# Optimization experiments

Hardware: AMD Instinct MI355X
Metric: run time of the kernel (lower is better)

## Reference

```python
import jax, jax.numpy as jnp
import numpy as np

BIT_DEPTH = 8  # feature squeezing

def setup_inputs() -> dict:
    key = jax.random.key(0)
    ks = jax.random.split(key, 8)
    B, C, H, W = 8, 256, 64, 64
    Cq = C // 8
    x = jax.random.normal(ks[0], (B, C, H, W), dtype=jnp.float32)
    # 1x1 conv weights stored as [out, in] (kernel dims squeezed)
    wq = jax.random.normal(ks[1], (Cq, C), dtype=jnp.float32) * 0.05
    bq = jax.random.normal(ks[2], (Cq,), dtype=jnp.float32) * 0.05
    wk = jax.random.normal(ks[3], (Cq, C), dtype=jnp.float32) * 0.05
    bk = jax.random.normal(ks[4], (Cq,), dtype=jnp.float32) * 0.05
    wv = jax.random.normal(ks[5], (C, C), dtype=jnp.float32) * 0.05
    bv = jax.random.normal(ks[6], (C,), dtype=jnp.float32) * 0.05
    gamma = jax.random.normal(ks[7], (1,), dtype=jnp.float32) * 0.1
    return {"x": x, "wq": wq, "bq": bq, "wk": wk, "bk": bk, "wv": wv, "bv": bv, "gamma": gamma}

def reference(x, wq, bq, wk, bk, wv, bv, gamma):
    B, C, H, W = x.shape
    N = H * W
    xf = x.reshape(B, C, N)  # flatten spatial
    # 1x1 convs == per-pixel linear projections
    q = jnp.einsum('bcn,oc->bon', xf, wq) + bq[None, :, None]   # [B, C/8, N]
    k = jnp.einsum('bcn,oc->bon', xf, wk) + bk[None, :, None]   # [B, C/8, N]
    v = jnp.einsum('bcn,oc->bon', xf, wv) + bv[None, :, None]   # [B, C, N]
    energy = jnp.einsum('bcn,bcm->bnm', q, k)                   # [B, N, N] (no scaling, as in source)
    attn = jax.nn.softmax(energy, axis=-1)
    out = jnp.einsum('bcm,bnm->bcn', v, attn).reshape(B, C, H, W)
    out = gamma[0] * out + out               # gamma-scaled residual of attention output
    scale = jnp.float32(2 ** BIT_DEPTH)
    return jnp.floor(out * scale) / scale    # feature squeezing (bit_depth=8)
```

## Files before the change

kernel.cpp:

```cpp
#include <hip/hip_runtime.h>
#include <math.h>

namespace {
constexpr int BB = 8;
constexpr int CH = 256;
constexpr int CQ = 32;
constexpr int NN = 4096;
}

typedef float f32x4 __attribute__((ext_vector_type(4)));
typedef short bf16x8 __attribute__((ext_vector_type(8)));
typedef unsigned short us8 __attribute__((ext_vector_type(8)));

#define MFMA16(a, b, c) __builtin_amdgcn_mfma_f32_16x16x32_bf16(a, b, c, 0, 0, 0)

__device__ __forceinline__ unsigned short f2bf(float x) {
    unsigned int u = __float_as_uint(x);
    u += 0x7fffu + ((u >> 16) & 1u);
    return (unsigned short)(u >> 16);
}
__device__ __forceinline__ float bf2f(unsigned short h) {
    return __uint_as_float(((unsigned int)h) << 16);
}
__device__ __forceinline__ void gload16(const void* g, void* l) {
    __builtin_amdgcn_global_load_lds(
        (const __attribute__((address_space(1))) unsigned int*)g,
        (__attribute__((address_space(3))) unsigned int*)l, 16, 0, 0);
}

__global__ __launch_bounds__(256) void wsplit_kernel(
    const float* __restrict__ wq, const float* __restrict__ wk,
    const float* __restrict__ wv,
    unsigned short* __restrict__ wh, unsigned short* __restrict__ wl)
{
    int idx = blockIdx.x * 256 + threadIdx.x;
    float v;
    if (idx < 8192)       v = wq[idx];
    else if (idx < 16384) v = wk[idx - 8192];
    else                  v = wv[idx - 16384];
    unsigned short hi = f2bf(v);
    wh[idx] = hi;
    wl[idx] = f2bf(v - bf2f(hi));
}

__global__ __launch_bounds__(256) void transpose_kernel(
    const float* __restrict__ x,
    unsigned short* __restrict__ xh, unsigned short* __restrict__ xl)
{
    __shared__ float xf[64 * 68];
    __shared__ unsigned short hs[64 * 80];
    __shared__ unsigned short ls[64 * 80];
    const int t  = threadIdx.x;
    const int b  = blockIdx.x >> 8;
    const int tl = blockIdx.x & 255;
    const int c0 = (tl >> 6) * 64;
    const int n0 = (tl & 63) * 64;

    #pragma unroll
    for (int i = 0; i < 4; ++i) {
        int idx = i * 256 + t;
        int c = idx >> 4, nf = idx & 15;
        float4 v4 = *(const float4*)(x + ((size_t)(b * 256 + c0 + c)) * NN + n0 + nf * 4);
        *(float4*)(xf + c * 68 + nf * 4) = v4;
    }
    __syncthreads();

    const int n = t & 63;
    #pragma unroll
    for (int loop = 0; loop < 2; ++loop) {
        int chunk = (t >> 6) + 4 * loop;
        us8 h8, l8;
        #pragma unroll
        for (int j = 0; j < 8; ++j) {
            float v = xf[(chunk * 8 + j) * 68 + n];
            unsigned short hi = f2bf(v);
            h8[j] = hi;
            l8[j] = f2bf(v - bf2f(hi));
        }
        *(us8*)(hs + n * 80 + chunk * 8) = h8;
        *(us8*)(ls + n * 80 + chunk * 8) = l8;
    }
    __syncthreads();

    {
        int rn = t >> 2, piece = t & 3;
        size_t grow = ((size_t)(b * NN + n0 + rn)) * 256 + c0 + piece * 16;
        *(us8*)(xh + grow)     = *(const us8*)(hs + rn * 80 + piece * 16);
        *(us8*)(xh + grow + 8) = *(const us8*)(hs + rn * 80 + piece * 16 + 8);
        *(us8*)(xl + grow)     = *(const us8*)(ls + rn * 80 + piece * 16);
        *(us8*)(xl + grow + 8) = *(const us8*)(ls + rn * 80 + piece * 16 + 8);
    }
}

#define PJ_XL 32768
#define PJ_VE 16384
__global__ __launch_bounds__(256, 2) void proj_kernel(
    const unsigned short* __restrict__ xh, const unsigned short* __restrict__ xl,
    const unsigned short* __restrict__ wh, const unsigned short* __restrict__ wl,
    const float* __restrict__ bq, const float* __restrict__ bk,
    const float* __restrict__ bv,
    unsigned short* __restrict__ qh, unsigned short* __restrict__ ql,
    unsigned short* __restrict__ kh, unsigned short* __restrict__ kl,
    unsigned short* __restrict__ vt)
{
    __shared__ __align__(16) unsigned char smem[65536];
    const int t    = threadIdx.x;
    const int lane = t & 63;
    const int w    = t >> 6;
    const int l16  = lane & 15;
    const int quad = lane >> 4;
    const int b    = blockIdx.x >> 6;
    const int n0   = (blockIdx.x & 63) << 6;

    const unsigned char* xhB = (const unsigned char*)(xh + ((size_t)b * NN + n0) * 256);
    const unsigned char* xlB = (const unsigned char*)(xl + ((size_t)b * NN + n0) * 256);
    #pragma unroll
    for (int j = 0; j < 8; ++j) {
        int idx = j * 256 + t;
        int r = idx >> 5, cl = idx & 31;
        int cg = cl ^ (r & 7);
        gload16(xhB + (size_t)r * 512 + cg * 16, smem + idx * 16);
        gload16(xlB + (size_t)r * 512 + cg * 16, smem + PJ_XL + idx * 16);
    }
    __syncthreads();

    f32x4 acc[5][4] = {};
    #pragma unroll 1
    for (int kc = 0; kc < 8; ++kc) {
        bf16x8 ah[5], al[5];
        #pragma unroll
        for (int i = 0; i < 5; ++i) {
            int och = (w * 5 + i) * 16 + l16;
            ah[i] = *(const bf16x8*)(wh + och * 256 + kc * 32 + quad * 8);
            al[i] = *(const bf16x8*)(wl + och * 256 + kc * 32 + quad * 8);
        }
        #pragma unroll
        for (int nt = 0; nt < 4; ++nt) {
            int roff = (nt * 16 + l16) * 512 + (((kc * 4 + quad) ^ (l16 & 7)) * 16);
            bf16x8 bh = *(const bf16x8*)(smem + roff);
            bf16x8 bl = *(const bf16x8*)(smem + PJ_XL + roff);
            #pragma unroll
            for (int i = 0; i < 5; ++i) {
                acc[i][nt] = MFMA16(ah[i], bh, acc[i][nt]);
                acc[i][nt] = MFMA16(al[i], bh, acc[i][nt]);
                acc[i][nt] = MFMA16(ah[i], bl, acc[i][nt]);
            }
        }
    }
    __syncthreads();

    #pragma unroll
    for (int i = 0; i < 5; ++i) {
        int tile = w * 5 + i;
        if (tile < 4) {
            #pragma unroll
            for (int r = 0; r < 4; ++r) {
                int och = tile * 16 + quad * 4 + r;
                float bias = (och < 32) ? bq[och] : bk[och - 32];
                int arr = (och < 32) ? 0 : 2;
                int oq = och & 31;
                #pragma unroll
                for (int nt = 0; nt < 4; ++nt) {
                    float val = acc[i][nt][r] + bias;
                    unsigned short hi = f2bf(val);
                    unsigned short lo = f2bf(val - bf2f(hi));
                    *(unsigned short*)(smem + arr * 4096 + (nt * 16 + l16) * 64 + oq * 2) = hi;
                    *(unsigned short*)(smem + (arr + 1) * 4096 + (nt * 16 + l16) * 64 + oq * 2) = lo;
                }
            }
        } else {
            #pragma unroll
            for (int r = 0; r < 4; ++r) {
                int voch = tile * 16 + quad * 4 + r - 64;
                float bias = bv[voch];
                #pragma unroll
                for (int nt = 0; nt < 4; ++nt) {
                    *(unsigned short*)(smem + PJ_VE + voch * 136 + (nt * 16 + l16) * 2)
                        = f2bf(acc[i][nt][r] + bias);
                }
            }
        }
    }
    __syncthreads();

    {
        unsigned short* dsts[4] = { qh, ql, kh, kl };
        int arr = t >> 6, n = t & 63;
        unsigned short* dst = dsts[arr] + ((size_t)b * NN + n0 + n) * 32;
        #pragma unroll
        for (int i = 0; i < 4; ++i)
            *(us8*)(dst + i * 8) = *(const us8*)(smem + arr * 4096 + n * 64 + i * 16);
    }
    #pragma unroll
    for (int p = 0; p < 4; ++p) {
        int voch = p * 64 + (t >> 2), piece = t & 3;
        unsigned short* dst = vt + ((size_t)b * CH + voch) * NN + n0 + piece * 16;
        *(us8*)(dst)     = *(const us8*)(smem + PJ_VE + voch * 136 + piece * 32);
        *(us8*)(dst + 8) = *(const us8*)(smem + PJ_VE + voch * 136 + piece * 32 + 16);
    }
}

#define A_P0 0
#define A_P1 8192
#define A_V0 16384
#define A_V1 49152
#define A_SM 16384

__global__ __launch_bounds__(256, 2) void attn_kernel(
    const unsigned short* __restrict__ qh, const unsigned short* __restrict__ ql,
    const unsigned short* __restrict__ kh, const unsigned short* __restrict__ kl,
    const unsigned short* __restrict__ vt, const float* __restrict__ gptr,
    float* __restrict__ out)
{
    __shared__ __align__(16) unsigned char smem[81920];
    const int t    = threadIdx.x;
    const int lane = t & 63;
    const int w    = t >> 6;
    const int l16  = lane & 15;
    const int quad = lane >> 4;
    const int b    = blockIdx.x & 7;
    const int n0   = (blockIdx.x >> 3) << 6;

    bf16x8 qhA[4], qlA[4];
    #pragma unroll
    for (int qt = 0; qt < 4; ++qt) {
        size_t row = (size_t)b * NN + n0 + qt * 16 + l16;
        qhA[qt] = *(const bf16x8*)(qh + row * 32 + quad * 8);
        qlA[qt] = *(const bf16x8*)(ql + row * 32 + quad * 8);
    }

    const unsigned short* khbase = kh + ((size_t)b * NN + w * 16 + l16) * 32 + quad * 8;
    const unsigned short* klbase = kl + ((size_t)b * NN + w * 16 + l16) * 32 + quad * 8;
    const unsigned char*  vtB    = (const unsigned char*)(vt + (size_t)b * CH * NN);

    f32x4 acc[4][4] = {};
    float S[4][4] = {};

    bf16x8 kch = *(const bf16x8*)(khbase);
    bf16x8 kcl = *(const bf16x8*)(klbase);
    #pragma unroll
    for (int j = 0; j < 8; ++j) {
        int idx = j * 256 + t;
        int r = idx >> 3, cl = idx & 7;
        int cg = cl ^ (r & 7);
        gload16(vtB + (size_t)r * 8192 + cg * 16, smem + A_V0 + idx * 16);
    }

    #pragma unroll 1
    for (int tile = 0; tile < 64; ++tile) {
        unsigned char* P = smem + ((tile & 1) ? A_P1 : A_P0);
        const int key = w * 16 + l16;
        #pragma unroll
        for (int qt = 0; qt < 4; ++qt) {
            f32x4 e = { 0.f, 0.f, 0.f, 0.f };
            e = MFMA16(qhA[qt], kch, e);
            e = MFMA16(qlA[qt], kch, e);
            e = MFMA16(qhA[qt], kcl, e);
            #pragma unroll
            for (int r = 0; r < 4; ++r) {
                float p = __expf(e[r]);
                unsigned short pb = f2bf(p);
                S[qt][r] += bf2f(pb);
                int row = qt * 16 + quad * 4 + r;
                *(unsigned short*)(P + row * 128
                                     + ((((key >> 3) ^ (row & 7)) << 4)
                                        | ((key & 7) << 1))) = pb;
            }
        }

        __syncthreads();

        const int m1 = ((tile + 1) & 63) * 64;
        bf16x8 knh = *(const bf16x8*)(khbase + (size_t)m1 * 32);
        bf16x8 knl = *(const bf16x8*)(klbase + (size_t)m1 * 32);
        if (tile < 63) {
            unsigned char* vdst = smem + ((tile & 1) ? A_V0 : A_V1);
            const unsigned char* vsrc = vtB + (size_t)m1 * 2;
            #pragma unroll
            for (int j = 0; j < 8; ++j) {
                int idx = j * 256 + t;
                int r = idx >> 3, cl = idx & 7;
                int cg = cl ^ (r & 7);
                gload16(vsrc + (size_t)r * 8192 + cg * 16, vdst + idx * 16);
            }
        }

        const unsigned char* VB = smem + ((tile & 1) ? A_V1 : A_V0);
        #pragma unroll
        for (int ks = 0; ks < 2; ++ks) {
            bf16x8 af[4], bfr[4];
            #pragma unroll
            for (int qt = 0; qt < 4; ++qt) {
                int row = qt * 16 + l16;
                af[qt] = *(const bf16x8*)(P + row * 128
                                            + (((ks * 4 + quad) ^ (row & 7)) << 4));
            }
            #pragma unroll
            for (int ct = 0; ct < 4; ++ct) {
                int vrow = w * 64 + ct * 16 + l16;
                int ch = (ks * 4 + quad) ^ (l16 & 7);
                bfr[ct] = *(const bf16x8*)(VB + vrow * 128 + ch * 16);
            }
            __builtin_amdgcn_s_setprio(1);
            #pragma unroll
            for (int qt = 0; qt < 4; ++qt)
                #pragma unroll
                for (int ct = 0; ct < 4; ++ct)
                    acc[qt][ct] = MFMA16(af[qt], bfr[ct], acc[qt][ct]);
            __builtin_amdgcn_s_setprio(0);
        }
        kch = knh;
        kcl = knl;
    }

    #pragma unroll
    for (int mask = 1; mask <= 8; mask <<= 1)
        #pragma unroll
        for (int qt = 0; qt < 4; ++qt)
            #pragma unroll
            for (int r = 0; r < 4; ++r)
                S[qt][r] += __shfl_xor(S[qt][r], mask);
    float* SM = (float*)(smem + A_SM);
    if (l16 == 0) {
        #pragma unroll
        for (int qt = 0; qt < 4; ++qt)
            #pragma unroll
            for (int r = 0; r < 4; ++r)
                SM[w * 64 + qt * 16 + quad * 4 + r] = S[qt][r];
    }
    __syncthreads();

    const float g1 = 1.f + gptr[0];
    float* ob = out + (size_t)b * CH * NN;
    #pragma unroll
    for (int qt = 0; qt < 4; ++qt) {
        float is[4];
        #pragma unroll
        for (int r = 0; r < 4; ++r) {
            int qi = qt * 16 + quad * 4 + r;
            float Sf = SM[qi] + SM[64 + qi] + SM[128 + qi] + SM[192 + qi];
            is[r] = g1 / Sf;
        }
        #pragma unroll
        for (int ct = 0; ct < 4; ++ct) {
            float4 o4;
            o4.x = floorf(acc[qt][ct][0] * is[0] * 256.f) * 0.00390625f;
            o4.y = floorf(acc[qt][ct][1] * is[1] * 256.f) * 0.00390625f;
            o4.z = floorf(acc[qt][ct][2] * is[2] * 256.f) * 0.00390625f;
            o4.w = floorf(acc[qt][ct][3] * is[3] * 256.f) * 0.00390625f;
            *(float4*)(ob + (size_t)(w * 64 + ct * 16 + l16) * NN
                          + n0 + qt * 16 + quad * 4) = o4;
        }
    }
}

extern "C" void kernel_launch(void* const* d_in, const int* in_sizes, int n_in,
                              void* d_out, int out_size, void* d_ws, size_t ws_size,
                              hipStream_t stream) {
    const float* x  = (const float*)d_in[0];
    const float* wq = (const float*)d_in[1];
    const float* bq = (const float*)d_in[2];
    const float* wk = (const float*)d_in[3];
    const float* bk = (const float*)d_in[4];
    const float* wv = (const float*)d_in[5];
    const float* bv = (const float*)d_in[6];
    const float* gm = (const float*)d_in[7];
    float* out = (float*)d_out;

    unsigned short* ws = (unsigned short*)d_ws;
    const size_t XSZ = (size_t)BB * NN * 256;
    const size_t WSZ = 320 * 256;
    const size_t QSZ = (size_t)BB * NN * 32;
    unsigned short* xh = ws;
    unsigned short* xl = xh + XSZ;
    unsigned short* wh = xl + XSZ;
    unsigned short* wl = wh + WSZ;
    unsigned short* qh = wl + WSZ;
    unsigned short* ql = qh + QSZ;
    unsigned short* kh = ql + QSZ;
    unsigned short* kl = kh + QSZ;
    unsigned short* vt = kl + QSZ;

    wsplit_kernel<<<320, 256, 0, stream>>>(wq, wk, wv, wh, wl);
    transpose_kernel<<<2048, 256, 0, stream>>>(x, xh, xl);
    proj_kernel<<<512, 256, 0, stream>>>(xh, xl, wh, wl, bq, bk, bv,
                                         qh, ql, kh, kl, vt);
    attn_kernel<<<512, 256, 0, stream>>>(qh, ql, kh, kl, vt, gm, out);
}
```

Before: 246.2 us.

## Restructure attention kernel to 8 waves with 128-key tiles and single-buffered V

The attention kernel moves from 4 to 8 waves per block and processes 128 keys per tile, halving the loop count. V is single-buffered, with an extra barrier before the next prefetch, and the wider P/V tiles use a 16-way XOR swizzle. Q is pre-scaled by log2(e) in the projection so exp2f can replace __expf, and packed bf16 conversion now writes P as 8-byte stores with the operands swapped. This aims to cut per-tile overhead and instruction count, at the cost of lost V load/compute overlap and an added sync per tile.

```diff
diff --git a/kernel.cpp b/kernel.cpp
--- a/kernel.cpp
+++ b/kernel.cpp
@@ -13,6 +13,7 @@
 typedef unsigned short us8 __attribute__((ext_vector_type(8)));
 
 #define MFMA16(a, b, c) __builtin_amdgcn_mfma_f32_16x16x32_bf16(a, b, c, 0, 0, 0)
+#define LOG2E 1.4426950408889634f
 
 __device__ __forceinline__ unsigned short f2bf(float x) {
     unsigned int u = __float_as_uint(x);
@@ -162,6 +163,7 @@
                 #pragma unroll
                 for (int nt = 0; nt < 4; ++nt) {
                     float val = acc[i][nt][r] + bias;
+                    if (och < 32) val *= LOG2E;
                     unsigned short hi = f2bf(val);
                     unsigned short lo = f2bf(val - bf2f(hi));
                     *(unsigned short*)(smem + arr * 4096 + (nt * 16 + l16) * 64 + oq * 2) = hi;
@@ -200,13 +202,10 @@
     }
 }
 
-#define A_P0 0
-#define A_P1 8192
-#define A_V0 16384
-#define A_V1 49152
-#define A_SM 16384
-
-__global__ __launch_bounds__(256, 2) void attn_kernel(
+#define A_P  0
+#define A_V  16384
+
+__global__ __launch_bounds__(512, 4) void attn_kernel(
     const unsigned short* __restrict__ qh, const unsigned short* __restrict__ ql,
     const unsigned short* __restrict__ kh, const unsigned short* __restrict__ kl,
     const unsigned short* __restrict__ vt, const float* __restrict__ gptr,
@@ -233,100 +232,95 @@
     const unsigned short* klbase = kl + ((size_t)b * NN + w * 16 + l16) * 32 + quad * 8;
     const unsigned char*  vtB    = (const unsigned char*)(vt + (size_t)b * CH * NN);
 
-    f32x4 acc[4][4] = {};
-    float S[4][4] = {};
+    f32x4 acc[4][2] = {};
+    float S[4] = {};
 
     bf16x8 kch = *(const bf16x8*)(khbase);
     bf16x8 kcl = *(const bf16x8*)(klbase);
     #pragma unroll
     for (int j = 0; j < 8; ++j) {
-        int idx = j * 256 + t;
-        int r = idx >> 3, cl = idx & 7;
-        int cg = cl ^ (r & 7);
-        gload16(vtB + (size_t)r * 8192 + cg * 16, smem + A_V0 + idx * 16);
-    }
-
+        int idx = j * 512 + t;
+        int r = idx >> 4, cl = idx & 15;
+        int cg = cl ^ (r & 15);
+        gload16(vtB + (size_t)r * 8192 + cg * 16, smem + A_V + idx * 16);
+    }
+
+    unsigned char* P = smem + A_P;
     #pragma unroll 1
-    for (int tile = 0; tile < 64; ++tile) {
-        unsigned char* P = smem + ((tile & 1) ? A_P1 : A_P0);
-        const int key = w * 16 + l16;
+    for (int tile = 0; tile < 32; ++tile) {
         #pragma unroll
         for (int qt = 0; qt < 4; ++qt) {
             f32x4 e = { 0.f, 0.f, 0.f, 0.f };
-            e = MFMA16(qhA[qt], kch, e);
-            e = MFMA16(qlA[qt], kch, e);
-            e = MFMA16(qhA[qt], kcl, e);
-            #pragma unroll
-            for (int r = 0; r < 4; ++r) {
-                float p = __expf(e[r]);
-                unsigned short pb = f2bf(p);
-                S[qt][r] += bf2f(pb);
-                int row = qt * 16 + quad * 4 + r;
-                *(unsigned short*)(P + row * 128
-                                     + ((((key >> 3) ^ (row & 7)) << 4)
-                                        | ((key & 7) << 1))) = pb;
-            }
-        }
-
+            e = MFMA16(kch, qhA[qt], e);
+            e = MFMA16(kch, qlA[qt], e);
+            e = MFMA16(kcl, qhA[qt], e);
+            float p0 = exp2f(e[0]), p1 = exp2f(e[1]);
+            float p2 = exp2f(e[2]), p3 = exp2f(e[3]);
+            unsigned int u01, u23;
+            asm("v_cvt_pk_bf16_f32 %0, %1, %2" : "=v"(u01) : "v"(p0), "v"(p1));
+            asm("v_cvt_pk_bf16_f32 %0, %1, %2" : "=v"(u23) : "v"(p2), "v"(p3));
+            S[qt] += (__uint_as_float(u01 << 16) + __uint_as_float(u01 & 0xffff0000u))
+                   + (__uint_as_float(u23 << 16) + __uint_as_float(u23 & 0xffff0000u));
+            int row = qt * 16 + l16;
+            int chunk = ((w << 1) | (quad >> 1)) ^ l16;
+            int2 pk2 = { (int)u01, (int)u23 };
+            *(int2*)(P + row * 256 + (chunk << 4) + ((quad & 1) << 3)) = pk2;
+        }
         __syncthreads();
 
-        const int m1 = ((tile + 1) & 63) * 64;
+        const int m1 = ((tile + 1) & 31) * 128;
         bf16x8 knh = *(const bf16x8*)(khbase + (size_t)m1 * 32);
         bf16x8 knl = *(const bf16x8*)(klbase + (size_t)m1 * 32);
-        if (tile < 63) {
-            unsigned char* vdst = smem + ((tile & 1) ? A_V0 : A_V1);
-            const unsigned char* vsrc = vtB + (size_t)m1 * 2;
-            #pragma unroll
-            for (int j = 0; j < 8; ++j) {
-                int idx = j * 256 + t;
-                int r = idx >> 3, cl = idx & 7;
-                int cg = cl ^ (r & 7);
-                gload16(vsrc + (size_t)r * 8192 + cg * 16, vdst + idx * 16);
-            }
-        }
-
-        const unsigned char* VB = smem + ((tile & 1) ? A_V1 : A_V0);
-        #pragma unroll
-        for (int ks = 0; ks < 2; ++ks) {
-            bf16x8 af[4], bfr[4];
+
+        #pragma unroll
+        for (int ks = 0; ks < 4; ++ks) {
+            bf16x8 af[4], bfr[2];
             #pragma unroll
             for (int qt = 0; qt < 4; ++qt) {
                 int row = qt * 16 + l16;
-                af[qt] = *(const bf16x8*)(P + row * 128
-                                            + (((ks * 4 + quad) ^ (row & 7)) << 4));
-            }
-            #pragma unroll
-            for (int ct = 0; ct < 4; ++ct) {
-                int vrow = w * 64 + ct * 16 + l16;
-                int ch = (ks * 4 + quad) ^ (l16 & 7);
-                bfr[ct] = *(const bf16x8*)(VB + vrow * 128 + ch * 16);
+                af[qt] = *(const bf16x8*)(P + row * 256
+                                            + ((((ks * 4 + quad) ^ l16)) << 4));
+            }
+            #pragma unroll
+            for (int ct = 0; ct < 2; ++ct) {
+                int vrow = w * 32 + ct * 16 + l16;
+                bfr[ct] = *(const bf16x8*)(smem + A_V + vrow * 256
+                                               + ((((ks * 4 + quad) ^ l16)) << 4));
             }
             __builtin_amdgcn_s_setprio(1);
             #pragma unroll
             for (int qt = 0; qt < 4; ++qt)
                 #pragma unroll
-                for (int ct = 0; ct < 4; ++ct)
+                for (int ct = 0; ct < 2; ++ct)
                     acc[qt][ct] = MFMA16(af[qt], bfr[ct], acc[qt][ct]);
             __builtin_amdgcn_s_setprio(0);
         }
+        __syncthreads();
+
+        if (tile < 31) {
+            const unsigned char* vsrc = vtB + (size_t)m1 * 2;
+            #pragma unroll
+            for (int j = 0; j < 8; ++j) {
+                int idx = j * 512 + t;
+                int r = idx >> 4, cl = idx & 15;
+                int cg = cl ^ (r & 15);
+                gload16(vsrc + (size_t)r * 8192 + cg * 16, smem + A_V + idx * 16);
+            }
+        }
         kch = knh;
         kcl = knl;
     }
 
     #pragma unroll
-    for (int mask = 1; mask <= 8; mask <<= 1)
+    for (int mask = 16; mask <= 32; mask <<= 1)
         #pragma unroll
         for (int qt = 0; qt < 4; ++qt)
-            #pragma unroll
-            for (int r = 0; r < 4; ++r)
-                S[qt][r] += __shfl_xor(S[qt][r], mask);
-    float* SM = (float*)(smem + A_SM);
-    if (l16 == 0) {
+            S[qt] += __shfl_xor(S[qt], mask);
+    float* SM = (float*)smem;
+    if (quad == 0) {
         #pragma unroll
         for (int qt = 0; qt < 4; ++qt)
-            #pragma unroll
-            for (int r = 0; r < 4; ++r)
-                SM[w * 64 + qt * 16 + quad * 4 + r] = S[qt][r];
+            SM[w * 64 + qt * 16 + l16] = S[qt];
     }
     __syncthreads();
 
@@ -338,17 +332,20 @@
         #pragma unroll
         for (int r = 0; r < 4; ++r) {
             int qi = qt * 16 + quad * 4 + r;
-            float Sf = SM[qi] + SM[64 + qi] + SM[128 + qi] + SM[192 + qi];
+            float Sf = 0.f;
+            #pragma unroll
+            for (int w8 = 0; w8 < 8; ++w8)
+                Sf += SM[w8 * 64 + qi];
             is[r] = g1 / Sf;
         }
         #pragma unroll
-        for (int ct = 0; ct < 4; ++ct) {
+        for (int ct = 0; ct < 2; ++ct) {
             float4 o4;
             o4.x = floorf(acc[qt][ct][0] * is[0] * 256.f) * 0.00390625f;
             o4.y = floorf(acc[qt][ct][1] * is[1] * 256.f) * 0.00390625f;
             o4.z = floorf(acc[qt][ct][2] * is[2] * 256.f) * 0.00390625f;
             o4.w = floorf(acc[qt][ct][3] * is[3] * 256.f) * 0.00390625f;
-            *(float4*)(ob + (size_t)(w * 64 + ct * 16 + l16) * NN
+            *(float4*)(ob + (size_t)(w * 32 + ct * 16 + l16) * NN
                           + n0 + qt * 16 + quad * 4) = o4;
         }
     }
@@ -385,5 +382,5 @@
     transpose_kernel<<<2048, 256, 0, stream>>>(x, xh, xl);
     proj_kernel<<<512, 256, 0, stream>>>(xh, xl, wh, wl, bq, bk, bv,
                                          qh, ql, kh, kl, vt);
-    attn_kernel<<<512, 256, 0, stream>>>(qh, ql, kh, kl, vt, gm, out);
-}
+    attn_kernel<<<512, 512, 0, stream>>>(qh, ql, kh, kl, vt, gm, out);
+}
```

New measurement: 347.8 us. 41.3% more time.

## Transpose energy MFMA, fold log2e into Q, pack P writes with cvt_pk_bf16

Applied to the files above, without the earlier changes.

Swaps the MFMA operands so each lane holds four consecutive keys for a single query row. This lets the exp'd probabilities be packed two at a time with v_cvt_pk_bf16_f32 and written to LDS as one 8-byte store instead of four 2-byte stores. log2e is folded into the Q projection so exp2f replaces __expf. The row-sum reduction shrinks to two cross-quad shuffles over 4 values, and the V prefetch addresses are precomputed and advanced by a constant. The intent is to cut VALU and LDS-store work in the softmax inner loop; the cost is slightly different rounding, from pre-scaling Q and from the hardware bf16 conversion.

```diff
diff --git a/kernel.cpp b/kernel.cpp
--- a/kernel.cpp
+++ b/kernel.cpp
@@ -13,6 +13,7 @@
 typedef unsigned short us8 __attribute__((ext_vector_type(8)));
 
 #define MFMA16(a, b, c) __builtin_amdgcn_mfma_f32_16x16x32_bf16(a, b, c, 0, 0, 0)
+#define LOG2E 1.4426950408889634f
 
 __device__ __forceinline__ unsigned short f2bf(float x) {
     unsigned int u = __float_as_uint(x);
@@ -162,6 +163,7 @@
                 #pragma unroll
                 for (int nt = 0; nt < 4; ++nt) {
                     float val = acc[i][nt][r] + bias;
+                    if (och < 32) val *= LOG2E;
                     unsigned short hi = f2bf(val);
                     unsigned short lo = f2bf(val - bf2f(hi));
                     *(unsigned short*)(smem + arr * 4096 + (nt * 16 + l16) * 64 + oq * 2) = hi;
@@ -233,39 +235,46 @@
     const unsigned short* klbase = kl + ((size_t)b * NN + w * 16 + l16) * 32 + quad * 8;
     const unsigned char*  vtB    = (const unsigned char*)(vt + (size_t)b * CH * NN);
 
-    f32x4 acc[4][4] = {};
-    float S[4][4] = {};
-
-    bf16x8 kch = *(const bf16x8*)(khbase);
-    bf16x8 kcl = *(const bf16x8*)(klbase);
+    const unsigned char* vsrc[8];
+    int vlds[8];
     #pragma unroll
     for (int j = 0; j < 8; ++j) {
         int idx = j * 256 + t;
         int r = idx >> 3, cl = idx & 7;
         int cg = cl ^ (r & 7);
-        gload16(vtB + (size_t)r * 8192 + cg * 16, smem + A_V0 + idx * 16);
-    }
+        vsrc[j] = vtB + (size_t)r * 8192 + cg * 16;
+        vlds[j] = idx * 16;
+    }
+    const int poff = l16 * 128 + ((((w << 1) | (quad >> 1)) ^ (l16 & 7)) << 4)
+                   + ((quad & 1) << 3);
+
+    f32x4 acc[4][4] = {};
+    float S[4] = {};
+
+    bf16x8 kch = *(const bf16x8*)(khbase);
+    bf16x8 kcl = *(const bf16x8*)(klbase);
+    #pragma unroll
+    for (int j = 0; j < 8; ++j)
+        gload16(vsrc[j], smem + A_V0 + vlds[j]);
 
     #pragma unroll 1
     for (int tile = 0; tile < 64; ++tile) {
         unsigned char* P = smem + ((tile & 1) ? A_P1 : A_P0);
-        const int key = w * 16 + l16;
         #pragma unroll
         for (int qt = 0; qt < 4; ++qt) {
             f32x4 e = { 0.f, 0.f, 0.f, 0.f };
-            e = MFMA16(qhA[qt], kch, e);
-            e = MFMA16(qlA[qt], kch, e);
-            e = MFMA16(qhA[qt], kcl, e);
-            #pragma unroll
-            for (int r = 0; r < 4; ++r) {
-                float p = __expf(e[r]);
-                unsigned short pb = f2bf(p);
-                S[qt][r] += bf2f(pb);
-                int row = qt * 16 + quad * 4 + r;
-                *(unsigned short*)(P + row * 128
-                                     + ((((key >> 3) ^ (row & 7)) << 4)
-                                        | ((key & 7) << 1))) = pb;
-            }
+            e = MFMA16(kch, qhA[qt], e);
+            e = MFMA16(kch, qlA[qt], e);
+            e = MFMA16(kcl, qhA[qt], e);
+            float p0 = exp2f(e[0]), p1 = exp2f(e[1]);
+            float p2 = exp2f(e[2]), p3 = exp2f(e[3]);
+            unsigned int u01, u23;
+            asm("v_cvt_pk_bf16_f32 %0, %1, %2" : "=v"(u01) : "v"(p0), "v"(p1));
+            asm("v_cvt_pk_bf16_f32 %0, %1, %2" : "=v"(u23) : "v"(p2), "v"(p3));
+            S[qt] += (__uint_as_float(u01 << 16) + __uint_as_float(u01 & 0xffff0000u))
+                   + (__uint_as_float(u23 << 16) + __uint_as_float(u23 & 0xffff0000u));
+            int2 pk2 = { (int)u01, (int)u23 };
+            *(int2*)(P + qt * 2048 + poff) = pk2;
         }
 
         __syncthreads();
@@ -275,13 +284,10 @@
         bf16x8 knl = *(const bf16x8*)(klbase + (size_t)m1 * 32);
         if (tile < 63) {
             unsigned char* vdst = smem + ((tile & 1) ? A_V0 : A_V1);
-            const unsigned char* vsrc = vtB + (size_t)m1 * 2;
             #pragma unroll
             for (int j = 0; j < 8; ++j) {
-                int idx = j * 256 + t;
-                int r = idx >> 3, cl = idx & 7;
-                int cg = cl ^ (r & 7);
-                gload16(vsrc + (size_t)r * 8192 + cg * 16, vdst + idx * 16);
+                vsrc[j] += 128;
+                gload16(vsrc[j], vdst + vlds[j]);
             }
         }
 
@@ -293,13 +299,13 @@
             for (int qt = 0; qt < 4; ++qt) {
                 int row = qt * 16 + l16;
                 af[qt] = *(const bf16x8*)(P + row * 128
-                                            + (((ks * 4 + quad) ^ (row & 7)) << 4));
+                                            + (((ks * 4 + quad) ^ (l16 & 7)) << 4));
             }
             #pragma unroll
             for (int ct = 0; ct < 4; ++ct) {
                 int vrow = w * 64 + ct * 16 + l16;
-                int ch = (ks * 4 + quad) ^ (l16 & 7);
-                bfr[ct] = *(const bf16x8*)(VB + vrow * 128 + ch * 16);
+                bfr[ct] = *(const bf16x8*)(VB + vrow * 128
+                                              + (((ks * 4 + quad) ^ (l16 & 7)) << 4));
             }
             __builtin_amdgcn_s_setprio(1);
             #pragma unroll
@@ -314,19 +320,15 @@
     }
 
     #pragma unroll
-    for (int mask = 1; mask <= 8; mask <<= 1)
+    for (int mask = 16; mask <= 32; mask <<= 1)
         #pragma unroll
         for (int qt = 0; qt < 4; ++qt)
-            #pragma unroll
-            for (int r = 0; r < 4; ++r)
-                S[qt][r] += __shfl_xor(S[qt][r], mask);
+            S[qt] += __shfl_xor(S[qt], mask);
     float* SM = (float*)(smem + A_SM);
-    if (l16 == 0) {
+    if (quad == 0) {
         #pragma unroll
         for (int qt = 0; qt < 4; ++qt)
-            #pragma unroll
-            for (int r = 0; r < 4; ++r)
-                SM[w * 64 + qt * 16 + quad * 4 + r] = S[qt][r];
+            SM[w * 64 + qt * 16 + l16] = S[qt];
     }
     __syncthreads();
 
```

Result: faster. 239.6 us (-2.7%).
